# Kernel tuning notes

Measured on AMD Instinct MI355X. Metric: run time of the kernel, lower is better.

Reference implementation:

```python
import jax, jax.numpy as jnp
import numpy as np

DIM = 768
N_HEAD = 12
HEAD_DIM = 64
INNER = N_HEAD * HEAD_DIM
SCALE = HEAD_DIM ** -0.5


def setup_inputs() -> dict:
    key = jax.random.key(0)
    ks = jax.random.split(key, 12)
    B, Sf, St = 4, 2048, 2048
    from_tensor = jax.random.normal(ks[0], (B, Sf, DIM), dtype=jnp.float32)
    to_tensor = jax.random.normal(ks[1], (B, St, DIM), dtype=jnp.float32)
    attention_mask = jax.random.randint(ks[2], (B, Sf, St), 0, 2, dtype=jnp.int32)
    # Dense layers: kernel ~ RandomNormal (stddev 0.05, keras default), bias zeros
    def kern(k, fan_in, fan_out):
        return 0.05 * jax.random.normal(k, (fan_in, fan_out), dtype=jnp.float32)
    return {
        "from_tensor": from_tensor,
        "to_tensor": to_tensor,
        "attention_mask": attention_mask,
        "Wq": kern(ks[3], DIM, INNER), "bq": jnp.zeros((INNER,), jnp.float32),
        "Wk": kern(ks[4], DIM, INNER), "bk": jnp.zeros((INNER,), jnp.float32),
        "Wv": kern(ks[5], DIM, INNER), "bv": jnp.zeros((INNER,), jnp.float32),
        "Wo": kern(ks[6], INNER, DIM), "bo": jnp.zeros((DIM,), jnp.float32),
    }


def reference(from_tensor, to_tensor, attention_mask, Wq, bq, Wk, bk, Wv, bv, Wo, bo):
    B, Sf, _ = from_tensor.shape
    St = to_tensor.shape[1]
    # projections -> [B, S, n_head, head_dim] -> [B, n_head, S, head_dim]
    def split_heads(x, S):
        return x.reshape(B, S, N_HEAD, HEAD_DIM).transpose(0, 2, 1, 3)
    q = split_heads(from_tensor @ Wq + bq, Sf) * SCALE
    k = split_heads(to_tensor @ Wk + bk, St)
    v = split_heads(to_tensor @ Wv + bv, St)
    # scores [B, H, Sf, St]
    scores = jnp.einsum('bhik,bhjk->bhij', q, k)
    adder = (1.0 - attention_mask.astype(jnp.float32)) * -10000.0
    scores = scores + adder[:, None, :, :]
    probs = jax.nn.softmax(scores, axis=-1)
    out = jnp.einsum('bhij,bhjk->bhik', probs, v)  # [B, H, Sf, Dh]
    out = out.transpose(0, 2, 1, 3).reshape(B, Sf, INNER)
    return out @ Wo + bo
```

## Files before the change

kernel.cpp:

```cpp
#include <hip/hip_runtime.h>
#include <stdint.h>

#define DIM 768
#define NH 12
#define HD 64
#define BSZ 4
#define SEQ 2048
#define MROWS (BSZ*SEQ)

typedef __attribute__((ext_vector_type(8))) short v8s;
typedef __attribute__((ext_vector_type(4))) float v4f;
typedef __attribute__((ext_vector_type(8))) _Float16 v8h;
typedef __attribute__((ext_vector_type(2))) __fp16 v2fp;

__device__ __forceinline__ uint16_t f2bf(float x) {
  union { float f; uint32_t u; } v; v.f = x;
  uint32_t r = v.u + 0x7fffu + ((v.u >> 16) & 1u);
  return (uint16_t)(r >> 16);
}

#if __has_builtin(__builtin_amdgcn_cvt_pk_bf16_f32)
typedef __attribute__((ext_vector_type(2))) __bf16 v2bf;
__device__ __forceinline__ uint32_t pack_bf16(float a, float b) {
  union { v2bf v; uint32_t u; } c;
  c.v = __builtin_amdgcn_cvt_pk_bf16_f32(a, b);
  return c.u;
}
#else
__device__ __forceinline__ uint32_t pack_bf16(float a, float b) {
  return (uint32_t)f2bf(a) | ((uint32_t)f2bf(b) << 16);
}
#endif

__device__ __forceinline__ uint32_t pack_f16(float a, float b) {
#if __has_builtin(__builtin_amdgcn_cvt_pkrtz)
  union { v2fp h; uint32_t u; } c;
  c.h = __builtin_amdgcn_cvt_pkrtz(a, b);
  return c.u;
#else
  union { _Float16 h[2]; uint32_t u; } c;
  c.h[0] = (_Float16)a; c.h[1] = (_Float16)b; return c.u;
#endif
}

__device__ __forceinline__ float fexp2(float x) {
#if __has_builtin(__builtin_amdgcn_exp2f)
  return __builtin_amdgcn_exp2f(x);
#else
  return exp2f(x);
#endif
}

__device__ __forceinline__ void gl16(const void* g, void* l) {
  __builtin_amdgcn_global_load_lds(
      (const __attribute__((address_space(1))) unsigned int*)g,
      (__attribute__((address_space(3))) unsigned int*)l, 16, 0, 0);
}

__global__ void cvt_bf16_kernel(const float* __restrict__ src0, uint16_t* __restrict__ dst0,
                                const float* __restrict__ src1, uint16_t* __restrict__ dst1,
                                int n4) {
  int i = blockIdx.x * blockDim.x + threadIdx.x;
  const float* src = (i < n4) ? src0 : src1;
  uint16_t* dst = (i < n4) ? dst0 : dst1;
  int j = (i < n4) ? i : i - n4;
  float4 v = ((const float4*)src)[j];
  ushort4 o;
  o.x = f2bf(v.x); o.y = f2bf(v.y); o.z = f2bf(v.z); o.w = f2bf(v.w);
  ((ushort4*)dst)[j] = o;
}

__global__ void mask_bits_kernel(const int* __restrict__ src,
                                 unsigned long long* __restrict__ dst, int nwords) {
  int gtid = blockIdx.x * blockDim.x + threadIdx.x;
  int w = gtid >> 6;
  int lane = threadIdx.x & 63;
  if (w >= nwords) return;
  int b  = w >> 16;
  int q  = (w >> 5) & 2047;
  int kt = w & 31;
  int m = src[((size_t)b * SEQ + q) * SEQ + kt * 64 + lane];
  unsigned long long bits = __ballot(m != 0);
  if (lane == 0) dst[((size_t)b * 32 + kt) * SEQ + q] = bits;
}

__global__ void wtrans_kernel(const float* __restrict__ Wq, const float* __restrict__ Wk,
                              const float* __restrict__ Wv, const float* __restrict__ Wo,
                              uint16_t* __restrict__ WT) {
  __shared__ float tile[32][33];
  int z = blockIdx.z;
  const float* src = (z==0) ? Wq : (z==1) ? Wk : (z==2) ? Wv : Wo;
  uint16_t* dst = WT + (size_t)z * DIM * DIM;
  int tx = threadIdx.x, ty = threadIdx.y;
  int x  = blockIdx.x * 32 + tx;
  int y0 = blockIdx.y * 32;
  for (int j = ty; j < 32; j += 8)
    tile[j][tx] = src[(size_t)(y0 + j) * DIM + x];
  __syncthreads();
  int xo = y0 + tx;
  for (int j = ty; j < 32; j += 8)
    dst[(size_t)(blockIdx.x * 32 + j) * DIM + xo] = f2bf(tile[tx][j]);
}

__global__ __launch_bounds__(256) void gemm_kernel(
    const uint16_t* __restrict__ Xf, const uint16_t* __restrict__ Xt,
    const uint16_t* __restrict__ WT, const uint16_t* __restrict__ AO,
    const float* __restrict__ bq, const float* __restrict__ bk,
    const float* __restrict__ bv, const float* __restrict__ bo,
    uint16_t* __restrict__ Qw, uint16_t* __restrict__ Kw, uint16_t* __restrict__ Vw,
    float* __restrict__ Out, int mode_base)
{
  __shared__ alignas(16) uint16_t As[128 * 32];
  __shared__ alignas(16) uint16_t Bs[128 * 32];
  int mode = mode_base + blockIdx.z;
  const uint16_t* A = (mode == 0) ? Xf : (mode == 3 ? AO : Xt);
  const uint16_t* W = WT + (size_t)mode * DIM * DIM;
  const float* bias = (mode == 0) ? bq : (mode == 1) ? bk : (mode == 2) ? bv : bo;

  int m0 = blockIdx.x * 128, n0 = blockIdx.y * 128;
  int tid = threadIdx.x;
  int wave = tid >> 6, lane = tid & 63, lr = lane & 15, quad = lane >> 4;
  int wm = (wave >> 1) * 64, wn = (wave & 1) * 64;

  int seg = (lane & 3) ^ ((lane >> 3) & 3);
  const uint16_t* agl = A + (size_t)(m0 + wave * 32 + (lane >> 2)) * DIM + seg * 8;
  const uint16_t* bgl = W + (size_t)(n0 + wave * 32 + (lane >> 2)) * DIM + seg * 8;
  int lb = wave * 1024;
  int ck = (lr >> 1) & 3;

  v4f acc[4][4];
  v4f vz = {0.f, 0.f, 0.f, 0.f};
  #pragma unroll
  for (int i = 0; i < 4; i++)
    #pragma unroll
    for (int j = 0; j < 4; j++) acc[i][j] = vz;

  for (int k0 = 0; k0 < DIM; k0 += 32) {
    __syncthreads();
    gl16(agl + k0,            &As[lb]);
    gl16(agl + k0 + 16 * DIM, &As[lb + 512]);
    gl16(bgl + k0,            &Bs[lb]);
    gl16(bgl + k0 + 16 * DIM, &Bs[lb + 512]);
    __syncthreads();
    v8s af[4], bfr[4];
    #pragma unroll
    for (int i = 0; i < 4; i++)
      af[i] = *(const v8s*)&As[(wm + i * 16 + lr) * 32 + ((quad ^ ck) << 3)];
    #pragma unroll
    for (int j = 0; j < 4; j++)
      bfr[j] = *(const v8s*)&Bs[(wn + j * 16 + lr) * 32 + ((quad ^ ck) << 3)];
    #pragma unroll
    for (int i = 0; i < 4; i++)
      #pragma unroll
      for (int j = 0; j < 4; j++)
        acc[i][j] = __builtin_amdgcn_mfma_f32_16x16x32_bf16(af[i], bfr[j], acc[i][j], 0, 0, 0);
  }

  float bj[4];
  #pragma unroll
  for (int j = 0; j < 4; j++) bj[j] = bias[n0 + wn + j * 16 + lr];

  if (mode == 3) {
    #pragma unroll
    for (int i = 0; i < 4; i++) {
      int m = m0 + wm + i * 16 + quad * 4;
      #pragma unroll
      for (int j = 0; j < 4; j++) {
        int n = n0 + wn + j * 16 + lr;
        #pragma unroll
        for (int r = 0; r < 4; r++)
          Out[(size_t)(m + r) * DIM + n] = acc[i][j][r] + bj[j];
      }
    }
  } else if (mode == 2) {
    #pragma unroll
    for (int i = 0; i < 4; i++) {
      int m = m0 + wm + i * 16 + quad * 4;
      int b = m >> 11, s0 = m & 2047;
      int kk0 = s0 & 63;
      int pos = (kk0 >> 5) * 32 + ((kk0 >> 2) & 3) * 8 + ((kk0 >> 4) & 1) * 4;
      int chunk = pos >> 3, off = pos & 7;
      #pragma unroll
      for (int j = 0; j < 4; j++) {
        int n = n0 + wn + j * 16 + lr;
        int h = n >> 6, d = n & 63;
        uint2 pk;
        pk.x = pack_f16(acc[i][j][0] + bj[j], acc[i][j][1] + bj[j]);
        pk.y = pack_f16(acc[i][j][2] + bj[j], acc[i][j][3] + bj[j]);
        int idx = (s0 & ~63) + ((chunk ^ (d & 7)) << 3) + off;
        *(uint2*)&Vw[((size_t)(b * NH + h) * HD + d) * SEQ + idx] = pk;
      }
    }
  } else {
    uint16_t* Dst = (mode == 0) ? Qw : Kw;
    float scale = (mode == 0) ? 0.18033688f : 1.0f;
    #pragma unroll
    for (int i = 0; i < 4; i++) {
      int m = m0 + wm + i * 16 + quad * 4;
      int b = m >> 11, s0 = m & 2047;
      #pragma unroll
      for (int j = 0; j < 4; j++) {
        int n = n0 + wn + j * 16 + lr;
        int h = n >> 6, d = n & 63;
        #pragma unroll
        for (int r = 0; r < 4; r++) {
          float v = (acc[i][j][r] + bj[j]) * scale;
          int s = s0 + r;
          int dd = (mode == 1) ? ((((d >> 3) ^ (s & 7)) << 3) + (d & 7)) : d;
          Dst[((size_t)(b * NH + h) * SEQ + s) * HD + dd] = f2bf(v);
        }
      }
    }
  }
}

__device__ __forceinline__ void softmax8(unsigned long long mw, int sh0,
                                         const v4f* s, v8h* pf, float& lsum) {
  uint32_t mlo = (uint32_t)mw, mhi = (uint32_t)(mw >> 32);
  #pragma unroll
  for (int p = 0; p < 2; p++) {
    float ps[8];
    #pragma unroll
    for (int half = 0; half < 2; half++) {
      int nt = p * 2 + half;
      uint32_t b4 = ((nt < 2 ? mlo : mhi) >> (sh0 + ((nt & 1) << 4))) & 15u;
      #pragma unroll
      for (int r = 0; r < 4; r++) {
        float v = fexp2(s[nt][r] - 8.0f) * (float)((b4 >> r) & 1u);
        ps[half * 4 + r] = v;
        lsum += v;
      }
    }
    union { uint4 u; v8h h; } cc;
    cc.u.x = pack_f16(ps[0], ps[1]);
    cc.u.y = pack_f16(ps[2], ps[3]);
    cc.u.z = pack_f16(ps[4], ps[5]);
    cc.u.w = pack_f16(ps[6], ps[7]);
    pf[p] = cc.h;
  }
}

__global__ __launch_bounds__(128, 3) void flash_kernel(
    const uint16_t* __restrict__ Qg, const uint16_t* __restrict__ Kg,
    const uint16_t* __restrict__ Vg, const unsigned long long* __restrict__ Mb,
    uint16_t* __restrict__ AO)
{
  __shared__ alignas(16) uint16_t Ks[64 * 64];
  __shared__ alignas(16) uint16_t Vs[64 * 64];

  int tid = threadIdx.x, wave = tid >> 6, lane = tid & 63, lr = lane & 15, quad = lane >> 4;
  int bh = blockIdx.y;
  int b = bh / NH, h = bh - b * NH;
  int q0 = blockIdx.x * 64;
  const uint16_t* Qp = Qg + (size_t)bh * SEQ * HD;
  const uint16_t* Kp = Kg + (size_t)bh * SEQ * HD;
  const uint16_t* Vp = Vg + (size_t)bh * HD * SEQ;
  int qg0 = q0 + wave * 32 + lr;
  int qg1 = qg0 + 16;
  const unsigned long long* Mp0 = Mb + (size_t)b * 32 * SEQ + qg0;
  const unsigned long long* Mp1 = Mp0 + 16;

  int swk = lr & 7, sh0 = quad * 4;

  v8s qf0a = *(const v8s*)&Qp[(size_t)qg0 * HD + quad * 8];
  v8s qf0b = *(const v8s*)&Qp[(size_t)qg0 * HD + 32 + quad * 8];
  v8s qf1a = *(const v8s*)&Qp[(size_t)qg1 * HD + quad * 8];
  v8s qf1b = *(const v8s*)&Qp[(size_t)qg1 * HD + 32 + quad * 8];

  const uint16_t* kgl = Kp + ((size_t)(wave * 32 + (lane >> 3)) * HD + (lane & 7) * 8);
  const uint16_t* vgl = Vp + ((size_t)(wave * 32 + (lane >> 3)) * SEQ + (lane & 7) * 8);
  int lb = wave * 2048;

  v4f acc0[4], acc1[4];
  v4f vz = {0.f, 0.f, 0.f, 0.f};
  #pragma unroll
  for (int dt = 0; dt < 4; dt++) { acc0[dt] = vz; acc1[dt] = vz; }
  float ls0 = 0.f, ls1 = 0.f;

  for (int k0 = 0; k0 < SEQ; k0 += 64) {
    __syncthreads();
    #pragma unroll
    for (int c = 0; c < 4; c++) {
      gl16(kgl + ((size_t)k0 + c * 8) * HD, &Ks[lb + c * 512]);
      gl16(vgl + k0 + (size_t)c * 8 * SEQ, &Vs[lb + c * 512]);
    }
    unsigned long long mw0 = Mp0[(size_t)(k0 >> 6) * SEQ];
    unsigned long long mw1 = Mp1[(size_t)(k0 >> 6) * SEQ];
    __syncthreads();

    v4f s0[4], s1[4];
    #pragma unroll
    for (int nt = 0; nt < 4; nt++) {
      int rowb = (nt * 16 + lr) << 6;
      v8s kf0 = *(const v8s*)&Ks[rowb + ((quad ^ swk) << 3)];
      v8s kf1 = *(const v8s*)&Ks[rowb + (((quad + 4) ^ swk) << 3)];
      v4f z = vz;
      z = __builtin_amdgcn_mfma_f32_16x16x32_bf16(kf0, qf0a, z, 0, 0, 0);
      z = __builtin_amdgcn_mfma_f32_16x16x32_bf16(kf1, qf0b, z, 0, 0, 0);
      s0[nt] = z;
      z = vz;
      z = __builtin_amdgcn_mfma_f32_16x16x32_bf16(kf0, qf1a, z, 0, 0, 0);
      z = __builtin_amdgcn_mfma_f32_16x16x32_bf16(kf1, qf1b, z, 0, 0, 0);
      s1[nt] = z;
    }

    v8h pf0[2], pf1[2];
    softmax8(mw0, sh0, s0, pf0, ls0);
    softmax8(mw1, sh0, s1, pf1, ls1);

    #pragma unroll
    for (int dt = 0; dt < 4; dt++) {
      int rowb = (dt * 16 + lr) << 6;
      #pragma unroll
      for (int p = 0; p < 2; p++) {
        v8h vv = *(const v8h*)&Vs[rowb + (((p * 4 + quad) ^ swk) << 3)];
        acc0[dt] = __builtin_amdgcn_mfma_f32_16x16x32_f16(vv, pf0[p], acc0[dt], 0, 0, 0);
        acc1[dt] = __builtin_amdgcn_mfma_f32_16x16x32_f16(vv, pf1[p], acc1[dt], 0, 0, 0);
      }
    }
  }

  ls0 += __shfl_xor(ls0, 16); ls0 += __shfl_xor(ls0, 32);
  ls1 += __shfl_xor(ls1, 16); ls1 += __shfl_xor(ls1, 32);
  float ri0 = 1.0f / ls0, ri1 = 1.0f / ls1;

  #pragma unroll
  for (int dt = 0; dt < 4; dt++) {
    uint2 pk;
    pk.x = pack_bf16(acc0[dt][0] * ri0, acc0[dt][1] * ri0);
    pk.y = pack_bf16(acc0[dt][2] * ri0, acc0[dt][3] * ri0);
    *(uint2*)&AO[(size_t)(b * SEQ + qg0) * DIM + h * HD + dt * 16 + sh0] = pk;
    pk.x = pack_bf16(acc1[dt][0] * ri1, acc1[dt][1] * ri1);
    pk.y = pack_bf16(acc1[dt][2] * ri1, acc1[dt][3] * ri1);
    *(uint2*)&AO[(size_t)(b * SEQ + qg1) * DIM + h * HD + dt * 16 + sh0] = pk;
  }
}

extern "C" void kernel_launch(void* const* d_in, const int* in_sizes, int n_in,
                              void* d_out, int out_size, void* d_ws, size_t ws_size,
                              hipStream_t stream) {
  const float* from_t = (const float*)d_in[0];
  const float* to_t   = (const float*)d_in[1];
  const int*   maski  = (const int*)d_in[2];
  const float* Wq = (const float*)d_in[3];  const float* bq = (const float*)d_in[4];
  const float* Wk = (const float*)d_in[5];  const float* bk = (const float*)d_in[6];
  const float* Wv = (const float*)d_in[7];  const float* bv = (const float*)d_in[8];
  const float* Wo = (const float*)d_in[9];  const float* bo = (const float*)d_in[10];

  char* ws = (char*)d_ws;
  size_t off = 0;
  uint16_t* Xf = (uint16_t*)(ws + off); off += (size_t)MROWS * DIM * 2;
  uint16_t* Xt = (uint16_t*)(ws + off); off += (size_t)MROWS * DIM * 2;
  uint16_t* WT = (uint16_t*)(ws + off); off += (size_t)4 * DIM * DIM * 2;
  unsigned long long* Mbits = (unsigned long long*)(ws + off);
  off += (size_t)BSZ * 32 * SEQ * 8;
  uint16_t* Qw = (uint16_t*)(ws + off); off += (size_t)MROWS * DIM * 2;
  uint16_t* Kw = (uint16_t*)(ws + off); off += (size_t)MROWS * DIM * 2;
  uint16_t* Vw = (uint16_t*)(ws + off); off += (size_t)MROWS * DIM * 2;
  uint16_t* AO = (uint16_t*)(ws + off); off += (size_t)MROWS * DIM * 2;
  float* Out = (float*)d_out;

  int nx4 = MROWS * DIM / 4;
  cvt_bf16_kernel<<<2 * nx4 / 256, 256, 0, stream>>>(from_t, Xf, to_t, Xt, nx4);
  int nwords = BSZ * 32 * SEQ;
  mask_bits_kernel<<<nwords * 64 / 256, 256, 0, stream>>>(maski, Mbits, nwords);
  wtrans_kernel<<<dim3(24, 24, 4), dim3(32, 8), 0, stream>>>(Wq, Wk, Wv, Wo, WT);

  gemm_kernel<<<dim3(64, 6, 3), 256, 0, stream>>>(Xf, Xt, WT, AO, bq, bk, bv, bo,
                                                  Qw, Kw, Vw, Out, 0);
  flash_kernel<<<dim3(SEQ / 64, BSZ * NH), 128, 0, stream>>>(Qw, Kw, Vw, Mbits, AO);
  gemm_kernel<<<dim3(64, 6, 1), 256, 0, stream>>>(Xf, Xt, WT, AO, bq, bk, bv, bo,
                                                  Qw, Kw, Vw, Out, 3);
}
```

Before: 330.1 us.

## Split flash block into four waves of 16 queries, MFMA row-sum, bias-folded exp

The flash kernel now uses 256 threads with each wave owning 16 query rows instead of 32, so K/V tiles in LDS are shared by four waves and occupancy is higher. The softmax row sum is computed with an MFMA against a ones vector rather than per-lane adds and shuffles. The -8 exponent offset is folded into the MFMA accumulator init. Register pressure per wave drops, but each wave does less work per LDS load and the sum is accumulated from fp16-rounded probabilities.

New measurement: 327.2 us. No clear change (-0.9%).

```diff
diff --git a/kernel.cpp b/kernel.cpp
--- a/kernel.cpp
+++ b/kernel.cpp
@@ -214,33 +214,7 @@
   }
 }
 
-__device__ __forceinline__ void softmax8(unsigned long long mw, int sh0,
-                                         const v4f* s, v8h* pf, float& lsum) {
-  uint32_t mlo = (uint32_t)mw, mhi = (uint32_t)(mw >> 32);
-  #pragma unroll
-  for (int p = 0; p < 2; p++) {
-    float ps[8];
-    #pragma unroll
-    for (int half = 0; half < 2; half++) {
-      int nt = p * 2 + half;
-      uint32_t b4 = ((nt < 2 ? mlo : mhi) >> (sh0 + ((nt & 1) << 4))) & 15u;
-      #pragma unroll
-      for (int r = 0; r < 4; r++) {
-        float v = fexp2(s[nt][r] - 8.0f) * (float)((b4 >> r) & 1u);
-        ps[half * 4 + r] = v;
-        lsum += v;
-      }
-    }
-    union { uint4 u; v8h h; } cc;
-    cc.u.x = pack_f16(ps[0], ps[1]);
-    cc.u.y = pack_f16(ps[2], ps[3]);
-    cc.u.z = pack_f16(ps[4], ps[5]);
-    cc.u.w = pack_f16(ps[6], ps[7]);
-    pf[p] = cc.h;
-  }
-}
-
-__global__ __launch_bounds__(128, 3) void flash_kernel(
+__global__ __launch_bounds__(256, 6) void flash_kernel(
     const uint16_t* __restrict__ Qg, const uint16_t* __restrict__ Kg,
     const uint16_t* __restrict__ Vg, const unsigned long long* __restrict__ Mb,
     uint16_t* __restrict__ AO)
@@ -255,58 +229,73 @@
   const uint16_t* Qp = Qg + (size_t)bh * SEQ * HD;
   const uint16_t* Kp = Kg + (size_t)bh * SEQ * HD;
   const uint16_t* Vp = Vg + (size_t)bh * HD * SEQ;
-  int qg0 = q0 + wave * 32 + lr;
-  int qg1 = qg0 + 16;
-  const unsigned long long* Mp0 = Mb + (size_t)b * 32 * SEQ + qg0;
-  const unsigned long long* Mp1 = Mp0 + 16;
+  int qg = q0 + wave * 16 + lr;
+  const unsigned long long* Mp = Mb + (size_t)b * 32 * SEQ + qg;
 
   int swk = lr & 7, sh0 = quad * 4;
 
-  v8s qf0a = *(const v8s*)&Qp[(size_t)qg0 * HD + quad * 8];
-  v8s qf0b = *(const v8s*)&Qp[(size_t)qg0 * HD + 32 + quad * 8];
-  v8s qf1a = *(const v8s*)&Qp[(size_t)qg1 * HD + quad * 8];
-  v8s qf1b = *(const v8s*)&Qp[(size_t)qg1 * HD + 32 + quad * 8];
-
-  const uint16_t* kgl = Kp + ((size_t)(wave * 32 + (lane >> 3)) * HD + (lane & 7) * 8);
-  const uint16_t* vgl = Vp + ((size_t)(wave * 32 + (lane >> 3)) * SEQ + (lane & 7) * 8);
-  int lb = wave * 2048;
-
-  v4f acc0[4], acc1[4];
+  v8s qfa = *(const v8s*)&Qp[(size_t)qg * HD + quad * 8];
+  v8s qfb = *(const v8s*)&Qp[(size_t)qg * HD + 32 + quad * 8];
+
+  const uint16_t* kgl = Kp + ((size_t)(wave * 16 + (lane >> 3)) * HD + (lane & 7) * 8);
+  const uint16_t* vgl = Vp + ((size_t)(wave * 16 + (lane >> 3)) * SEQ + (lane & 7) * 8);
+  int lb = wave * 1024;
+
+  v8h ones;
+  #pragma unroll
+  for (int i = 0; i < 8; i++) ones[i] = (_Float16)1.0f;
+
+  v4f acc[4], lacc;
   v4f vz = {0.f, 0.f, 0.f, 0.f};
-  #pragma unroll
-  for (int dt = 0; dt < 4; dt++) { acc0[dt] = vz; acc1[dt] = vz; }
-  float ls0 = 0.f, ls1 = 0.f;
+  v4f m8 = {-8.f, -8.f, -8.f, -8.f};
+  #pragma unroll
+  for (int dt = 0; dt < 4; dt++) acc[dt] = vz;
+  lacc = vz;
 
   for (int k0 = 0; k0 < SEQ; k0 += 64) {
     __syncthreads();
-    #pragma unroll
-    for (int c = 0; c < 4; c++) {
-      gl16(kgl + ((size_t)k0 + c * 8) * HD, &Ks[lb + c * 512]);
-      gl16(vgl + k0 + (size_t)c * 8 * SEQ, &Vs[lb + c * 512]);
-    }
-    unsigned long long mw0 = Mp0[(size_t)(k0 >> 6) * SEQ];
-    unsigned long long mw1 = Mp1[(size_t)(k0 >> 6) * SEQ];
+    gl16(kgl + (size_t)k0 * HD,       &Ks[lb]);
+    gl16(kgl + (size_t)(k0 + 8) * HD, &Ks[lb + 512]);
+    gl16(vgl + k0,                    &Vs[lb]);
+    gl16(vgl + k0 + (size_t)8 * SEQ,  &Vs[lb + 512]);
+    unsigned long long mw = Mp[(size_t)(k0 >> 6) * SEQ];
     __syncthreads();
 
-    v4f s0[4], s1[4];
-    #pragma unroll
-    for (int nt = 0; nt < 4; nt++) {
-      int rowb = (nt * 16 + lr) << 6;
-      v8s kf0 = *(const v8s*)&Ks[rowb + ((quad ^ swk) << 3)];
-      v8s kf1 = *(const v8s*)&Ks[rowb + (((quad + 4) ^ swk) << 3)];
-      v4f z = vz;
-      z = __builtin_amdgcn_mfma_f32_16x16x32_bf16(kf0, qf0a, z, 0, 0, 0);
-      z = __builtin_amdgcn_mfma_f32_16x16x32_bf16(kf1, qf0b, z, 0, 0, 0);
-      s0[nt] = z;
-      z = vz;
-      z = __builtin_amdgcn_mfma_f32_16x16x32_bf16(kf0, qf1a, z, 0, 0, 0);
-      z = __builtin_amdgcn_mfma_f32_16x16x32_bf16(kf1, qf1b, z, 0, 0, 0);
-      s1[nt] = z;
-    }
-
-    v8h pf0[2], pf1[2];
-    softmax8(mw0, sh0, s0, pf0, ls0);
-    softmax8(mw1, sh0, s1, pf1, ls1);
+    uint32_t mlo = (uint32_t)mw, mhi = (uint32_t)(mw >> 32);
+    v8h pf[2];
+    #pragma unroll
+    for (int p = 0; p < 2; p++) {
+      v4f sA = m8, sB = m8;
+      {
+        int rowb = ((2 * p) * 16 + lr) << 6;
+        v8s kf0 = *(const v8s*)&Ks[rowb + ((quad ^ swk) << 3)];
+        v8s kf1 = *(const v8s*)&Ks[rowb + (((quad + 4) ^ swk) << 3)];
+        sA = __builtin_amdgcn_mfma_f32_16x16x32_bf16(kf0, qfa, sA, 0, 0, 0);
+        sA = __builtin_amdgcn_mfma_f32_16x16x32_bf16(kf1, qfb, sA, 0, 0, 0);
+      }
+      {
+        int rowb = ((2 * p + 1) * 16 + lr) << 6;
+        v8s kf0 = *(const v8s*)&Ks[rowb + ((quad ^ swk) << 3)];
+        v8s kf1 = *(const v8s*)&Ks[rowb + (((quad + 4) ^ swk) << 3)];
+        sB = __builtin_amdgcn_mfma_f32_16x16x32_bf16(kf0, qfa, sB, 0, 0, 0);
+        sB = __builtin_amdgcn_mfma_f32_16x16x32_bf16(kf1, qfb, sB, 0, 0, 0);
+      }
+      uint32_t mword = p ? mhi : mlo;
+      uint32_t b4a = (mword >> sh0) & 15u;
+      uint32_t b4b = (mword >> (sh0 + 16)) & 15u;
+      float ps[8];
+      #pragma unroll
+      for (int r = 0; r < 4; r++) {
+        ps[r]     = fexp2(sA[r]) * (float)((b4a >> r) & 1u);
+        ps[4 + r] = fexp2(sB[r]) * (float)((b4b >> r) & 1u);
+      }
+      union { uint4 u; v8h h; } cc;
+      cc.u.x = pack_f16(ps[0], ps[1]);
+      cc.u.y = pack_f16(ps[2], ps[3]);
+      cc.u.z = pack_f16(ps[4], ps[5]);
+      cc.u.w = pack_f16(ps[6], ps[7]);
+      pf[p] = cc.h;
+    }
 
     #pragma unroll
     for (int dt = 0; dt < 4; dt++) {
@@ -314,25 +303,21 @@
       #pragma unroll
       for (int p = 0; p < 2; p++) {
         v8h vv = *(const v8h*)&Vs[rowb + (((p * 4 + quad) ^ swk) << 3)];
-        acc0[dt] = __builtin_amdgcn_mfma_f32_16x16x32_f16(vv, pf0[p], acc0[dt], 0, 0, 0);
-        acc1[dt] = __builtin_amdgcn_mfma_f32_16x16x32_f16(vv, pf1[p], acc1[dt], 0, 0, 0);
-      }
-    }
+        acc[dt] = __builtin_amdgcn_mfma_f32_16x16x32_f16(vv, pf[p], acc[dt], 0, 0, 0);
+      }
+    }
+    lacc = __builtin_amdgcn_mfma_f32_16x16x32_f16(ones, pf[0], lacc, 0, 0, 0);
+    lacc = __builtin_amdgcn_mfma_f32_16x16x32_f16(ones, pf[1], lacc, 0, 0, 0);
   }
 
-  ls0 += __shfl_xor(ls0, 16); ls0 += __shfl_xor(ls0, 32);
-  ls1 += __shfl_xor(ls1, 16); ls1 += __shfl_xor(ls1, 32);
-  float ri0 = 1.0f / ls0, ri1 = 1.0f / ls1;
+  float ri = 1.0f / lacc[0];
 
   #pragma unroll
   for (int dt = 0; dt < 4; dt++) {
     uint2 pk;
-    pk.x = pack_bf16(acc0[dt][0] * ri0, acc0[dt][1] * ri0);
-    pk.y = pack_bf16(acc0[dt][2] * ri0, acc0[dt][3] * ri0);
-    *(uint2*)&AO[(size_t)(b * SEQ + qg0) * DIM + h * HD + dt * 16 + sh0] = pk;
-    pk.x = pack_bf16(acc1[dt][0] * ri1, acc1[dt][1] * ri1);
-    pk.y = pack_bf16(acc1[dt][2] * ri1, acc1[dt][3] * ri1);
-    *(uint2*)&AO[(size_t)(b * SEQ + qg1) * DIM + h * HD + dt * 16 + sh0] = pk;
+    pk.x = pack_bf16(acc[dt][0] * ri, acc[dt][1] * ri);
+    pk.y = pack_bf16(acc[dt][2] * ri, acc[dt][3] * ri);
+    *(uint2*)&AO[(size_t)(b * SEQ + qg) * DIM + h * HD + dt * 16 + sh0] = pk;
   }
 }
 
@@ -368,7 +353,7 @@
 
   gemm_kernel<<<dim3(64, 6, 3), 256, 0, stream>>>(Xf, Xt, WT, AO, bq, bk, bv, bo,
                                                   Qw, Kw, Vw, Out, 0);
-  flash_kernel<<<dim3(SEQ / 64, BSZ * NH), 128, 0, stream>>>(Qw, Kw, Vw, Mbits, AO);
+  flash_kernel<<<dim3(SEQ / 64, BSZ * NH), 256, 0, stream>>>(Qw, Kw, Vw, Mbits, AO);
   gemm_kernel<<<dim3(64, 6, 1), 256, 0, stream>>>(Xf, Xt, WT, AO, bq, bk, bv, bo,
                                                   Qw, Kw, Vw, Out, 3);
 }
```
